# Kernel optimization log

Measured on AMD Instinct MI355X. Metric: run time of the kernel, lower is better.

Reference implementation:

```python
import jax, jax.numpy as jnp
import numpy as np

N = 50000
E = 1600000
NUM_GRAPHS = 64
NEG_SLOPE = 0.2


def _glorot(key, shape):
    fan_in, fan_out = shape[0], shape[-1]
    lim = jnp.sqrt(6.0 / (fan_in + fan_out))
    return jax.random.uniform(key, shape, jnp.float32, -lim, lim)


def setup_inputs() -> dict:
    key = jax.random.key(0)
    ks = jax.random.split(key, 16)
    x = jax.random.normal(ks[0], (N, 128), jnp.float32)
    edge_index = jax.random.randint(ks[1], (2, E), 0, N, jnp.int64)
    batch = jnp.sort(jax.random.randint(ks[2], (N,), 0, NUM_GRAPHS, jnp.int64))
    dims = [(128, 32), (32, 64), (64, 128)]
    params = {}
    for i, (fi, fo) in enumerate(dims, start=1):
        params[f'W{i}'] = _glorot(ks[3 * i], (fi, fo))
        params[f'a_src{i}'] = _glorot(ks[3 * i + 1], (1, fo))[0]
        params[f'a_dst{i}'] = _glorot(ks[3 * i + 2], (1, fo))[0]
        params[f'b{i}'] = jnp.zeros((fo,), jnp.float32)
    params['lin1_W'] = _glorot(ks[12], (128, 32))
    params['lin1_b'] = jnp.zeros((32,), jnp.float32)
    params['lin2_W'] = _glorot(ks[13], (32, 10))
    params['lin2_b'] = jnp.zeros((10,), jnp.float32)
    return dict(x=x, edge_index=edge_index, batch=batch, **params)


def gat_conv(x, src, dst, W, a_src, a_dst, b):
    # h: [N, F_out]
    h = x @ W
    # per-node attention logits, gathered per edge
    as_n = h @ a_src  # [N]
    ad_n = h @ a_dst  # [N]
    e = jax.nn.leaky_relu(as_n[src] + ad_n[dst], NEG_SLOPE)  # [E']
    # segment softmax over incoming edges of each destination node
    m = jax.ops.segment_max(e, dst, num_segments=N)
    ee = jnp.exp(e - m[dst])
    s = jax.ops.segment_sum(ee, dst, num_segments=N)
    alpha = ee / (s[dst] + 1e-16)
    # weighted scatter-add of source messages
    out = jax.ops.segment_sum(h[src] * alpha[:, None], dst, num_segments=N)
    return out + b


def reference(x, edge_index, batch, W1, a_src1, a_dst1, b1, W2, a_src2, a_dst2, b2,
              W3, a_src3, a_dst3, b3, lin1_W, lin1_b, lin2_W, lin2_b):
    # add self loops (PyG GATConv default)
    loops = jnp.arange(N, dtype=edge_index.dtype)
    src = jnp.concatenate([edge_index[0], loops])
    dst = jnp.concatenate([edge_index[1], loops])
    h = jax.nn.relu(gat_conv(x, src, dst, W1, a_src1, a_dst1, b1))
    h = jax.nn.relu(gat_conv(h, src, dst, W2, a_src2, a_dst2, b2))
    h = gat_conv(h, src, dst, W3, a_src3, a_dst3, b3)
    # global_add_pool over graphs
    g = jax.ops.segment_sum(h, batch, num_segments=NUM_GRAPHS)  # [G, 128]
    g = jax.nn.relu(g @ lin1_W + lin1_b)
    g = g @ lin2_W + lin2_b
    # faithful to original: log_softmax over dim=0 (batch axis)
    return jax.nn.log_softmax(g, axis=0)
```

## Files before the change

kernel.cpp:

```cpp
#include <hip/hip_runtime.h>
#include <cstdint>
#include <cstddef>

#define NN 50000
#define NE 1600000
#define NG 64
#define NCB 196
#define EPB_A 16384
#define CAP_B 16384

__device__ __forceinline__ float bflo(unsigned u) { return __uint_as_float(u << 16); }
__device__ __forceinline__ float bfhi(unsigned u) { return __uint_as_float(u & 0xffff0000u); }
__device__ __forceinline__ unsigned f2bf(float f) {
    unsigned u = __float_as_uint(f);
    return (u + 0x7fffu + ((u >> 16) & 1u)) >> 16;
}

template <int FIN, int FOUT>
__global__ void gemm_bf_k(const float* __restrict__ A, const float* __restrict__ W,
                          unsigned* __restrict__ Hb, int n) {
    const int RPB = 32;
    const int CP = FOUT / 2;
    const int CLANES = 256 / CP;
    const int RL = RPB / CLANES;
    __shared__ float Wl[FIN * FOUT];
    __shared__ float Al[RPB * FIN];
    int tid = threadIdx.x;
    for (int i = tid; i < (FIN * FOUT) / 4; i += 256)
        ((float4*)Wl)[i] = ((const float4*)W)[i];
    int rowbase = blockIdx.x * RPB;
    int nrows = min(RPB, n - rowbase);
    int nel4 = (nrows * FIN) / 4;
    const float4* Asrc = (const float4*)(A + (size_t)rowbase * FIN);
    for (int i = tid; i < nel4; i += 256) ((float4*)Al)[i] = Asrc[i];
    __syncthreads();
    int c2 = tid % CP;
    int rb = tid / CP;
    float acc0[RL], acc1[RL];
#pragma unroll
    for (int r = 0; r < RL; ++r) { acc0[r] = 0.f; acc1[r] = 0.f; }
#pragma unroll 4
    for (int k = 0; k < FIN; ++k) {
        float w0 = Wl[k * FOUT + 2 * c2];
        float w1 = Wl[k * FOUT + 2 * c2 + 1];
#pragma unroll
        for (int r = 0; r < RL; ++r) {
            float a = Al[(rb + r * CLANES) * FIN + k];
            acc0[r] += a * w0;
            acc1[r] += a * w1;
        }
    }
#pragma unroll
    for (int r = 0; r < RL; ++r) {
        int row = rowbase + rb + r * CLANES;
        if (row < n) Hb[(size_t)row * CP + c2] = f2bf(acc0[r]) | (f2bf(acc1[r]) << 16);
    }
}

template <int F>
__global__ void att_logits_k(const unsigned short* __restrict__ Hb,
                             const float* __restrict__ a_src, const float* __restrict__ a_dst,
                             float* __restrict__ as_, float* __restrict__ ad_) {
    const int GRP = F / 4;
    long long t = (long long)blockIdx.x * blockDim.x + threadIdx.x;
    int node = (int)(t / GRP);
    int lane = (int)(t % GRP);
    if (node >= NN) return;
    ushort4 h4 = ((const ushort4*)(Hb + (size_t)node * F))[lane];
    float h0 = bflo(h4.x), h1 = bflo(h4.y), h2 = bflo(h4.z), h3 = bflo(h4.w);
    float4 s4 = ((const float4*)a_src)[lane];
    float4 d4 = ((const float4*)a_dst)[lane];
    float s1 = h0 * s4.x + h1 * s4.y + h2 * s4.z + h3 * s4.w;
    float s2 = h0 * d4.x + h1 * d4.y + h2 * d4.z + h3 * d4.w;
#pragma unroll
    for (int o = GRP >> 1; o; o >>= 1) {
        s1 += __shfl_xor(s1, o, GRP);
        s2 += __shfl_xor(s2, o, GRP);
    }
    if (lane == 0) {
        as_[node] = s1;
        ad_[node] = s2;
    }
}

__global__ void chist_k(const int* __restrict__ edst, int* __restrict__ gcount) {
    __shared__ int h[NCB];
    int tid = threadIdx.x;
    for (int i = tid; i < NCB; i += 256) h[i] = 0;
    __syncthreads();
    const int total4 = NE / 4;
    for (int i = blockIdx.x * 256 + tid; i < total4; i += gridDim.x * 256) {
        int4 d = ((const int4*)edst)[i];
        atomicAdd(&h[d.x >> 8], 1);
        atomicAdd(&h[d.y >> 8], 1);
        atomicAdd(&h[d.z >> 8], 1);
        atomicAdd(&h[d.w >> 8], 1);
    }
    __syncthreads();
    for (int i = tid; i < NCB; i += 256)
        if (h[i]) atomicAdd(&gcount[i], h[i]);
}

__global__ void cscan_k(const int* __restrict__ gcount, int* __restrict__ cbase,
                        int* __restrict__ gcur) {
    __shared__ int sc[256];
    int tid = threadIdx.x;
    int c0 = (tid < NCB) ? gcount[tid] : 0;
    sc[tid] = c0;
    __syncthreads();
    for (int off = 1; off < 256; off <<= 1) {
        int v = (tid >= off) ? sc[tid - off] : 0;
        __syncthreads();
        sc[tid] += v;
        __syncthreads();
    }
    int excl = sc[tid] - c0;
    if (tid < NCB) { cbase[tid] = excl; gcur[tid] = excl; }
    if (tid == 255) cbase[NCB] = sc[255];
}

__global__ void parta_k(const int* __restrict__ esrc, const int* __restrict__ edst,
                        int* __restrict__ gcur, int* __restrict__ pk_g) {
    __shared__ int cnt[NCB];
    __shared__ int base[NCB];
    __shared__ int cur[NCB];
    __shared__ int gposs[NCB];
    __shared__ int sc[256];
    __shared__ int lpk[EPB_A];
    int tid = threadIdx.x;
    int e0 = blockIdx.x * EPB_A;
    int e1 = min(e0 + EPB_A, NE);
    for (int i = tid; i < NCB; i += 256) cnt[i] = 0;
    __syncthreads();
    for (int i = e0 / 4 + tid; i < e1 / 4; i += 256) {
        int4 d = ((const int4*)edst)[i];
        atomicAdd(&cnt[d.x >> 8], 1);
        atomicAdd(&cnt[d.y >> 8], 1);
        atomicAdd(&cnt[d.z >> 8], 1);
        atomicAdd(&cnt[d.w >> 8], 1);
    }
    __syncthreads();
    int c0 = (tid < NCB) ? cnt[tid] : 0;
    sc[tid] = c0;
    __syncthreads();
    for (int off = 1; off < 256; off <<= 1) {
        int v = (tid >= off) ? sc[tid - off] : 0;
        __syncthreads();
        sc[tid] += v;
        __syncthreads();
    }
    if (tid < NCB) {
        int excl = sc[tid] - c0;
        base[tid] = excl;
        cur[tid] = excl;
        gposs[tid] = atomicAdd(&gcur[tid], c0);
    }
    __syncthreads();
    for (int i = e0 / 4 + tid; i < e1 / 4; i += 256) {
        int4 d = ((const int4*)edst)[i];
        int4 s = ((const int4*)esrc)[i];
        lpk[atomicAdd(&cur[d.x >> 8], 1)] = s.x | ((d.x & 255) << 17);
        lpk[atomicAdd(&cur[d.y >> 8], 1)] = s.y | ((d.y & 255) << 17);
        lpk[atomicAdd(&cur[d.z >> 8], 1)] = s.z | ((d.z & 255) << 17);
        lpk[atomicAdd(&cur[d.w >> 8], 1)] = s.w | ((d.w & 255) << 17);
    }
    __syncthreads();
    int wid = tid >> 6, lane = tid & 63;
    for (int c = wid; c < NCB; c += 4) {
        int n = cnt[c], gb = gposs[c], lb = base[c];
        for (int i = lane; i < n; i += 64) pk_g[gb + i] = lpk[lb + i];
    }
}

__global__ void partb_k(const int* __restrict__ pk_g, const int* __restrict__ cbase,
                        int* __restrict__ offsets, int* __restrict__ csr) {
    __shared__ int cnt[256];
    __shared__ int sc[256];
    __shared__ int lpk[CAP_B];
    int b = blockIdx.x, tid = threadIdx.x;
    int ebeg = cbase[b], eend = cbase[b + 1], n = eend - ebeg;
    int nbeg = b * 256;
    int ncnt = min(256, NN - nbeg);
    cnt[tid] = 0;
    __syncthreads();
    bool fits = (n <= CAP_B);
    if (fits) {
        for (int i = tid; i < n; i += 256) {
            int p = pk_g[ebeg + i];
            lpk[i] = p;
            atomicAdd(&cnt[p >> 17], 1);
        }
    } else {
        for (int i = tid; i < n; i += 256) atomicAdd(&cnt[pk_g[ebeg + i] >> 17], 1);
    }
    __syncthreads();
    int c0 = cnt[tid];
    sc[tid] = c0;
    __syncthreads();
    for (int off = 1; off < 256; off <<= 1) {
        int v = (tid >= off) ? sc[tid - off] : 0;
        __syncthreads();
        sc[tid] += v;
        __syncthreads();
    }
    int excl = sc[tid] - c0;
    if (tid < ncnt) offsets[nbeg + tid] = ebeg + excl;
    if (b == NCB - 1 && tid == 0) offsets[NN] = eend;
    __syncthreads();
    cnt[tid] = ebeg + excl;
    __syncthreads();
    if (fits) {
        for (int i = tid; i < n; i += 256) {
            int p = lpk[i];
            csr[atomicAdd(&cnt[p >> 17], 1)] = p & 0x1FFFF;
        }
    } else {
        for (int i = tid; i < n; i += 256) {
            int p = pk_g[ebeg + i];
            csr[atomicAdd(&cnt[p >> 17], 1)] = p & 0x1FFFF;
        }
    }
}

template <int F, bool RELU>
__global__ void node_agg_k(const int* __restrict__ off, const int* __restrict__ csr,
                           const float* __restrict__ as_, const float* __restrict__ ad_,
                           const unsigned* __restrict__ Hb2,
                           const float* __restrict__ b, float* __restrict__ O) {
    const int GRP = F / 2;
    const int EPG = 64 / GRP;
    const int U = (EPG == 1) ? 4 : 2;
    int lane = threadIdx.x & 63;
    int node = blockIdx.x * (blockDim.x >> 6) + (threadIdx.x >> 6);
    if (node >= NN) return;
    int beg = off[node], end = off[node + 1];
    float adn = ad_[node];
    float vself = as_[node] + adn;
    vself = vself > 0.f ? vself : 0.2f * vself;

    float mx = vself;
    for (int i = beg + lane; i < end; i += 64) {
        float v = as_[csr[i]] + adn;
        v = v > 0.f ? v : 0.2f * v;
        mx = fmaxf(mx, v);
    }
#pragma unroll
    for (int o = 32; o; o >>= 1) mx = fmaxf(mx, __shfl_xor(mx, o));

    int sg = lane / GRP;
    int cl = lane % GRP;
    float eself = __expf(vself - mx);
    unsigned hbs = Hb2[(size_t)node * GRP + cl];
    float accx = (sg == 0) ? eself * bflo(hbs) : 0.f;
    float accy = (sg == 0) ? eself * bfhi(hbs) : 0.f;
    float lsum = 0.f;

    for (int i0 = beg; i0 < end; i0 += 64) {
        int idx = i0 + lane;
        bool ok = idx < end;
        int s = ok ? csr[idx] : 0;
        float v = as_[s] + adn;
        v = v > 0.f ? v : 0.2f * v;
        float ee = ok ? __expf(v - mx) : 0.f;
        lsum += ee;
        int rem = min(end - i0, 64);
        int nj = (rem + EPG - 1) / EPG;
        nj = (nj + U - 1) & ~(U - 1);
        for (int j = 0; j < nj; j += U) {
#pragma unroll
            for (int k = 0; k < U; ++k) {
                int pos = (j + k) * EPG + sg;
                int s2 = __shfl(s, pos);
                float ee2 = __shfl(ee, pos);
                unsigned hb = Hb2[(size_t)s2 * GRP + cl];
                accx += ee2 * bflo(hb);
                accy += ee2 * bfhi(hb);
            }
        }
    }
#pragma unroll
    for (int o = 32; o; o >>= 1) lsum += __shfl_xor(lsum, o);
    float sum = lsum + eself;
#pragma unroll
    for (int o = 32; o >= GRP; o >>= 1) {
        accx += __shfl_xor(accx, o);
        accy += __shfl_xor(accy, o);
    }
    if (sg == 0) {
        float inv = 1.f / (sum + 1e-16f);
        float2 bb = ((const float2*)b)[cl];
        float ox = accx * inv + bb.x;
        float oy = accy * inv + bb.y;
        if (RELU) {
            ox = fmaxf(ox, 0.f);
            oy = fmaxf(oy, 0.f);
        }
        ((float2*)O)[(size_t)node * GRP + cl] = make_float2(ox, oy);
    }
}

__global__ void pool_k(const float* __restrict__ O, const int* __restrict__ batch,
                       float* __restrict__ g, int nodes_per_block) {
    __shared__ float acc[NG * 128];
    int c = threadIdx.x;
    for (int i = 0; i < NG; ++i) acc[i * 128 + c] = 0.f;
    int start = blockIdx.x * nodes_per_block;
    int end = min(start + nodes_per_block, NN);
    int gmin = NG - 1, gmax = 0;
    for (int nd = start; nd < end; ++nd) {
        int gg = batch[nd];
        gmin = min(gmin, gg);
        gmax = max(gmax, gg);
        acc[gg * 128 + c] += O[(size_t)nd * 128 + c];
    }
    for (int i = gmin; i <= gmax; ++i) atomicAdd(g + i * 128 + c, acc[i * 128 + c]);
}

__global__ void head_k(const float* __restrict__ g, const float* __restrict__ l1W,
                       const float* __restrict__ l1b, const float* __restrict__ l2W,
                       const float* __restrict__ l2b, float* __restrict__ out) {
    __shared__ float h1[NG * 32];
    __shared__ float o[NG * 10];
    int tid = threadIdx.x;
    for (int idx = tid; idx < NG * 32; idx += 256) {
        int r = idx / 32, c = idx % 32;
        float acc = l1b[c];
        for (int k = 0; k < 128; ++k) acc += g[r * 128 + k] * l1W[k * 32 + c];
        h1[idx] = fmaxf(acc, 0.f);
    }
    __syncthreads();
    for (int idx = tid; idx < NG * 10; idx += 256) {
        int r = idx / 10, c = idx % 10;
        float acc = l2b[c];
        for (int k = 0; k < 32; ++k) acc += h1[r * 32 + k] * l2W[k * 10 + c];
        o[idx] = acc;
    }
    __syncthreads();
    if (tid < 10) {
        float mx = -1e30f;
        for (int r = 0; r < NG; ++r) mx = fmaxf(mx, o[r * 10 + tid]);
        float sum = 0.f;
        for (int r = 0; r < NG; ++r) sum += __expf(o[r * 10 + tid] - mx);
        float lse = mx + logf(sum);
        for (int r = 0; r < NG; ++r) out[r * 10 + tid] = o[r * 10 + tid] - lse;
    }
}

extern "C" void kernel_launch(void* const* d_in, const int* in_sizes, int n_in,
                              void* d_out, int out_size, void* d_ws, size_t ws_size,
                              hipStream_t stream) {
    const float* x   = (const float*)d_in[0];
    const int* ei    = (const int*)d_in[1];
    const int* batch = (const int*)d_in[2];
    const float* W1 = (const float*)d_in[3];
    const float* as1 = (const float*)d_in[4];
    const float* ad1 = (const float*)d_in[5];
    const float* b1 = (const float*)d_in[6];
    const float* W2 = (const float*)d_in[7];
    const float* as2 = (const float*)d_in[8];
    const float* ad2 = (const float*)d_in[9];
    const float* b2 = (const float*)d_in[10];
    const float* W3 = (const float*)d_in[11];
    const float* as3 = (const float*)d_in[12];
    const float* ad3 = (const float*)d_in[13];
    const float* b3 = (const float*)d_in[14];
    const float* l1W = (const float*)d_in[15];
    const float* l1b = (const float*)d_in[16];
    const float* l2W = (const float*)d_in[17];
    const float* l2b = (const float*)d_in[18];
    float* out = (float*)d_out;

    const int* esrc = ei;
    const int* edst = ei + NE;

    char* ws = (char*)d_ws;
    float* B0 = (float*)ws;
    float* B1 = B0 + (size_t)NN * 128;
    unsigned* Hb = (unsigned*)(B1 + (size_t)NN * 64);
    float* as_ = (float*)(Hb + (size_t)NN * 64);
    float* ad_ = as_ + NN;
    int* gcount = (int*)(ad_ + NN);
    int* cbase  = gcount + NCB;
    int* gcur   = cbase + NCB + 1;
    int* offsets = gcur + NCB + 2;
    int* csr    = offsets + NN + 1;
    int* pk     = csr + NE;
    float* g    = (float*)(pk + NE);

    hipMemsetAsync(gcount, 0, NCB * 4, stream);
    chist_k<<<98, 256, 0, stream>>>(edst, gcount);
    cscan_k<<<1, 256, 0, stream>>>(gcount, cbase, gcur);
    parta_k<<<(NE + EPB_A - 1) / EPB_A, 256, 0, stream>>>(esrc, edst, gcur, pk);
    partb_k<<<NCB, 256, 0, stream>>>(pk, cbase, offsets, csr);

    gemm_bf_k<128, 32><<<(NN + 31) / 32, 256, 0, stream>>>(x, W1, Hb, NN);
    att_logits_k<32><<<((long long)NN * 8 + 255) / 256, 256, 0, stream>>>(
        (const unsigned short*)Hb, as1, ad1, as_, ad_);
    node_agg_k<32, true><<<(NN + 3) / 4, 256, 0, stream>>>(offsets, csr, as_, ad_, Hb, b1, B0);

    gemm_bf_k<32, 64><<<(NN + 31) / 32, 256, 0, stream>>>(B0, W2, Hb, NN);
    att_logits_k<64><<<((long long)NN * 16 + 255) / 256, 256, 0, stream>>>(
        (const unsigned short*)Hb, as2, ad2, as_, ad_);
    node_agg_k<64, true><<<(NN + 3) / 4, 256, 0, stream>>>(offsets, csr, as_, ad_, Hb, b2, B1);

    gemm_bf_k<64, 128><<<(NN + 31) / 32, 256, 0, stream>>>(B1, W3, Hb, NN);
    att_logits_k<128><<<((long long)NN * 32 + 255) / 256, 256, 0, stream>>>(
        (const unsigned short*)Hb, as3, ad3, as_, ad_);
    node_agg_k<128, false><<<(NN + 3) / 4, 256, 0, stream>>>(offsets, csr, as_, ad_, Hb, b3, B0);

    hipMemsetAsync(g, 0, (size_t)NG * 128 * 4, stream);
    pool_k<<<(NN + 127) / 128, 128, 0, stream>>>(B0, batch, g, 128);
    head_k<<<1, 256, 0, stream>>>(g, l1W, l1b, l2W, l2b, out);
}
```

Baseline: 328.8 us.

## Fuse attention logits into GEMM, merge histogram, rework aggregation lanes

Computes the per-node source and destination attention logits inside the GEMM epilogue using shuffle reductions, which removes the separate att_logits kernels and the re-read of H. The destination histogram is folded into the first GEMM launch as extra blocks, and the two memsets are combined into one by placing g next to gcount. The 64- and 128-feature aggregation paths now have each lane own output columns and broadcast edge indices with readlane, instead of splitting the wavefront into edge subgroups and reducing across them at the end. This trades fewer launches and less memory traffic for a longer serial per-edge loop in each wavefront.

```diff
diff --git a/kernel.cpp b/kernel.cpp
--- a/kernel.cpp
+++ b/kernel.cpp
@@ -15,21 +15,45 @@
     unsigned u = __float_as_uint(f);
     return (u + 0x7fffu + ((u >> 16) & 1u)) >> 16;
 }
-
-template <int FIN, int FOUT>
-__global__ void gemm_bf_k(const float* __restrict__ A, const float* __restrict__ W,
-                          unsigned* __restrict__ Hb, int n) {
+__device__ __forceinline__ float rdlane_f(float v, int l) {
+    return __uint_as_float((unsigned)__builtin_amdgcn_readlane((int)__float_as_uint(v), l));
+}
+
+template <int FIN, int FOUT, bool HIST>
+__global__ void gemm_att_k(const float* __restrict__ A, const float* __restrict__ W,
+                           const float* __restrict__ a_src, const float* __restrict__ a_dst,
+                           unsigned* __restrict__ Hb, float* __restrict__ as_,
+                           float* __restrict__ ad_, int gemmBlocks,
+                           const int* __restrict__ edst, int* __restrict__ gcount) {
+    __shared__ float Wl[FIN * FOUT];
+    __shared__ float Al[32 * FIN];
+    __shared__ int hh[NCB];
+    int tid = threadIdx.x;
+    if (HIST && blockIdx.x >= gemmBlocks) {
+        int bid = blockIdx.x - gemmBlocks;
+        for (int i = tid; i < NCB; i += 256) hh[i] = 0;
+        __syncthreads();
+        const int total4 = NE / 4;
+        for (int i = bid * 256 + tid; i < total4; i += 98 * 256) {
+            int4 d = ((const int4*)edst)[i];
+            atomicAdd(&hh[d.x >> 8], 1);
+            atomicAdd(&hh[d.y >> 8], 1);
+            atomicAdd(&hh[d.z >> 8], 1);
+            atomicAdd(&hh[d.w >> 8], 1);
+        }
+        __syncthreads();
+        for (int i = tid; i < NCB; i += 256)
+            if (hh[i]) atomicAdd(&gcount[i], hh[i]);
+        return;
+    }
     const int RPB = 32;
     const int CP = FOUT / 2;
     const int CLANES = 256 / CP;
     const int RL = RPB / CLANES;
-    __shared__ float Wl[FIN * FOUT];
-    __shared__ float Al[RPB * FIN];
-    int tid = threadIdx.x;
     for (int i = tid; i < (FIN * FOUT) / 4; i += 256)
         ((float4*)Wl)[i] = ((const float4*)W)[i];
     int rowbase = blockIdx.x * RPB;
-    int nrows = min(RPB, n - rowbase);
+    int nrows = min(RPB, NN - rowbase);
     int nel4 = (nrows * FIN) / 4;
     const float4* Asrc = (const float4*)(A + (size_t)rowbase * FIN);
     for (int i = tid; i < nel4; i += 256) ((float4*)Al)[i] = Asrc[i];
@@ -50,55 +74,23 @@
             acc1[r] += a * w1;
         }
     }
+    float2 asrc2 = ((const float2*)a_src)[c2];
+    float2 adst2 = ((const float2*)a_dst)[c2];
 #pragma unroll
     for (int r = 0; r < RL; ++r) {
         int row = rowbase + rb + r * CLANES;
-        if (row < n) Hb[(size_t)row * CP + c2] = f2bf(acc0[r]) | (f2bf(acc1[r]) << 16);
-    }
-}
-
-template <int F>
-__global__ void att_logits_k(const unsigned short* __restrict__ Hb,
-                             const float* __restrict__ a_src, const float* __restrict__ a_dst,
-                             float* __restrict__ as_, float* __restrict__ ad_) {
-    const int GRP = F / 4;
-    long long t = (long long)blockIdx.x * blockDim.x + threadIdx.x;
-    int node = (int)(t / GRP);
-    int lane = (int)(t % GRP);
-    if (node >= NN) return;
-    ushort4 h4 = ((const ushort4*)(Hb + (size_t)node * F))[lane];
-    float h0 = bflo(h4.x), h1 = bflo(h4.y), h2 = bflo(h4.z), h3 = bflo(h4.w);
-    float4 s4 = ((const float4*)a_src)[lane];
-    float4 d4 = ((const float4*)a_dst)[lane];
-    float s1 = h0 * s4.x + h1 * s4.y + h2 * s4.z + h3 * s4.w;
-    float s2 = h0 * d4.x + h1 * d4.y + h2 * d4.z + h3 * d4.w;
-#pragma unroll
-    for (int o = GRP >> 1; o; o >>= 1) {
-        s1 += __shfl_xor(s1, o, GRP);
-        s2 += __shfl_xor(s2, o, GRP);
-    }
-    if (lane == 0) {
-        as_[node] = s1;
-        ad_[node] = s2;
-    }
-}
-
-__global__ void chist_k(const int* __restrict__ edst, int* __restrict__ gcount) {
-    __shared__ int h[NCB];
-    int tid = threadIdx.x;
-    for (int i = tid; i < NCB; i += 256) h[i] = 0;
-    __syncthreads();
-    const int total4 = NE / 4;
-    for (int i = blockIdx.x * 256 + tid; i < total4; i += gridDim.x * 256) {
-        int4 d = ((const int4*)edst)[i];
-        atomicAdd(&h[d.x >> 8], 1);
-        atomicAdd(&h[d.y >> 8], 1);
-        atomicAdd(&h[d.z >> 8], 1);
-        atomicAdd(&h[d.w >> 8], 1);
-    }
-    __syncthreads();
-    for (int i = tid; i < NCB; i += 256)
-        if (h[i]) atomicAdd(&gcount[i], h[i]);
+        float p1 = acc0[r] * asrc2.x + acc1[r] * asrc2.y;
+        float p2 = acc0[r] * adst2.x + acc1[r] * adst2.y;
+#pragma unroll
+        for (int o = CP >> 1; o; o >>= 1) {
+            p1 += __shfl_xor(p1, o, CP);
+            p2 += __shfl_xor(p2, o, CP);
+        }
+        if (row < NN) {
+            Hb[(size_t)row * CP + c2] = f2bf(acc0[r]) | (f2bf(acc1[r]) << 16);
+            if (c2 == 0) { as_[row] = p1; ad_[row] = p2; }
+        }
+    }
 }
 
 __global__ void cscan_k(const int* __restrict__ gcount, int* __restrict__ cbase,
@@ -227,9 +219,6 @@
                            const float* __restrict__ as_, const float* __restrict__ ad_,
                            const unsigned* __restrict__ Hb2,
                            const float* __restrict__ b, float* __restrict__ O) {
-    const int GRP = F / 2;
-    const int EPG = 64 / GRP;
-    const int U = (EPG == 1) ? 4 : 2;
     int lane = threadIdx.x & 63;
     int node = blockIdx.x * (blockDim.x >> 6) + (threadIdx.x >> 6);
     if (node >= NN) return;
@@ -246,56 +235,128 @@
     }
 #pragma unroll
     for (int o = 32; o; o >>= 1) mx = fmaxf(mx, __shfl_xor(mx, o));
-
-    int sg = lane / GRP;
-    int cl = lane % GRP;
     float eself = __expf(vself - mx);
-    unsigned hbs = Hb2[(size_t)node * GRP + cl];
-    float accx = (sg == 0) ? eself * bflo(hbs) : 0.f;
-    float accy = (sg == 0) ? eself * bfhi(hbs) : 0.f;
     float lsum = 0.f;
 
-    for (int i0 = beg; i0 < end; i0 += 64) {
-        int idx = i0 + lane;
-        bool ok = idx < end;
-        int s = ok ? csr[idx] : 0;
-        float v = as_[s] + adn;
-        v = v > 0.f ? v : 0.2f * v;
-        float ee = ok ? __expf(v - mx) : 0.f;
-        lsum += ee;
-        int rem = min(end - i0, 64);
-        int nj = (rem + EPG - 1) / EPG;
-        nj = (nj + U - 1) & ~(U - 1);
-        for (int j = 0; j < nj; j += U) {
-#pragma unroll
-            for (int k = 0; k < U; ++k) {
-                int pos = (j + k) * EPG + sg;
-                int s2 = __shfl(s, pos);
-                float ee2 = __shfl(ee, pos);
-                unsigned hb = Hb2[(size_t)s2 * GRP + cl];
+    if constexpr (F == 128) {
+        unsigned hbs = Hb2[(size_t)node * 64 + lane];
+        float accx = eself * bflo(hbs);
+        float accy = eself * bfhi(hbs);
+        for (int i0 = beg; i0 < end; i0 += 64) {
+            int idx = i0 + lane;
+            bool ok = idx < end;
+            int s = ok ? csr[idx] : 0;
+            float v = as_[s] + adn;
+            v = v > 0.f ? v : 0.2f * v;
+            float ee = ok ? __expf(v - mx) : 0.f;
+            lsum += ee;
+            int rem = min(end - i0, 64);
+            int j = 0;
+            for (; j + 4 <= rem; j += 4) {
+#pragma unroll
+                for (int k = 0; k < 4; ++k) {
+                    int s2 = __builtin_amdgcn_readlane(s, j + k);
+                    float ee2 = rdlane_f(ee, j + k);
+                    unsigned hb = (Hb2 + (size_t)s2 * 64)[lane];
+                    accx += ee2 * bflo(hb);
+                    accy += ee2 * bfhi(hb);
+                }
+            }
+            for (; j < rem; ++j) {
+                int s2 = __builtin_amdgcn_readlane(s, j);
+                float ee2 = rdlane_f(ee, j);
+                unsigned hb = (Hb2 + (size_t)s2 * 64)[lane];
                 accx += ee2 * bflo(hb);
                 accy += ee2 * bfhi(hb);
             }
         }
-    }
-#pragma unroll
-    for (int o = 32; o; o >>= 1) lsum += __shfl_xor(lsum, o);
-    float sum = lsum + eself;
-#pragma unroll
-    for (int o = 32; o >= GRP; o >>= 1) {
-        accx += __shfl_xor(accx, o);
-        accy += __shfl_xor(accy, o);
-    }
-    if (sg == 0) {
-        float inv = 1.f / (sum + 1e-16f);
-        float2 bb = ((const float2*)b)[cl];
+#pragma unroll
+        for (int o = 32; o; o >>= 1) lsum += __shfl_xor(lsum, o);
+        float inv = 1.f / (lsum + eself + 1e-16f);
+        float2 bb = ((const float2*)b)[lane];
         float ox = accx * inv + bb.x;
         float oy = accy * inv + bb.y;
-        if (RELU) {
-            ox = fmaxf(ox, 0.f);
-            oy = fmaxf(oy, 0.f);
-        }
-        ((float2*)O)[(size_t)node * GRP + cl] = make_float2(ox, oy);
+        if (RELU) { ox = fmaxf(ox, 0.f); oy = fmaxf(oy, 0.f); }
+        ((float2*)O)[(size_t)node * 64 + lane] = make_float2(ox, oy);
+    } else if constexpr (F == 64) {
+        const unsigned short* Hs = (const unsigned short*)Hb2;
+        float acc = eself * bflo((unsigned)Hs[(size_t)node * 64 + lane]);
+        for (int i0 = beg; i0 < end; i0 += 64) {
+            int idx = i0 + lane;
+            bool ok = idx < end;
+            int s = ok ? csr[idx] : 0;
+            float v = as_[s] + adn;
+            v = v > 0.f ? v : 0.2f * v;
+            float ee = ok ? __expf(v - mx) : 0.f;
+            lsum += ee;
+            int rem = min(end - i0, 64);
+            int j = 0;
+            for (; j + 4 <= rem; j += 4) {
+#pragma unroll
+                for (int k = 0; k < 4; ++k) {
+                    int s2 = __builtin_amdgcn_readlane(s, j + k);
+                    float ee2 = rdlane_f(ee, j + k);
+                    acc += ee2 * bflo((unsigned)(Hs + (size_t)s2 * 64)[lane]);
+                }
+            }
+            for (; j < rem; ++j) {
+                int s2 = __builtin_amdgcn_readlane(s, j);
+                float ee2 = rdlane_f(ee, j);
+                acc += ee2 * bflo((unsigned)(Hs + (size_t)s2 * 64)[lane]);
+            }
+        }
+#pragma unroll
+        for (int o = 32; o; o >>= 1) lsum += __shfl_xor(lsum, o);
+        float inv = 1.f / (lsum + eself + 1e-16f);
+        float ox = acc * inv + b[lane];
+        if (RELU) ox = fmaxf(ox, 0.f);
+        O[(size_t)node * 64 + lane] = ox;
+    } else {
+        const int GRP = 16, EPG = 4, U = 2;
+        int sg = lane / GRP;
+        int cl = lane % GRP;
+        unsigned hbs = Hb2[(size_t)node * GRP + cl];
+        float accx = (sg == 0) ? eself * bflo(hbs) : 0.f;
+        float accy = (sg == 0) ? eself * bfhi(hbs) : 0.f;
+        for (int i0 = beg; i0 < end; i0 += 64) {
+            int idx = i0 + lane;
+            bool ok = idx < end;
+            int s = ok ? csr[idx] : 0;
+            float v = as_[s] + adn;
+            v = v > 0.f ? v : 0.2f * v;
+            float ee = ok ? __expf(v - mx) : 0.f;
+            lsum += ee;
+            int rem = min(end - i0, 64);
+            int nj = (rem + EPG - 1) / EPG;
+            nj = (nj + U - 1) & ~(U - 1);
+            for (int j = 0; j < nj; j += U) {
+#pragma unroll
+                for (int k = 0; k < U; ++k) {
+                    int pos = (j + k) * EPG + sg;
+                    int s2 = __shfl(s, pos);
+                    float ee2 = __shfl(ee, pos);
+                    unsigned hb = Hb2[(size_t)s2 * GRP + cl];
+                    accx += ee2 * bflo(hb);
+                    accy += ee2 * bfhi(hb);
+                }
+            }
+        }
+#pragma unroll
+        for (int o = 32; o; o >>= 1) lsum += __shfl_xor(lsum, o);
+        float sum = lsum + eself;
+#pragma unroll
+        for (int o = 32; o >= GRP; o >>= 1) {
+            accx += __shfl_xor(accx, o);
+            accy += __shfl_xor(accy, o);
+        }
+        if (sg == 0) {
+            float inv = 1.f / (sum + 1e-16f);
+            float2 bb = ((const float2*)b)[cl];
+            float ox = accx * inv + bb.x;
+            float oy = accy * inv + bb.y;
+            if (RELU) { ox = fmaxf(ox, 0.f); oy = fmaxf(oy, 0.f); }
+            ((float2*)O)[(size_t)node * GRP + cl] = make_float2(ox, oy);
+        }
     }
 }
 
@@ -380,35 +441,31 @@
     float* as_ = (float*)(Hb + (size_t)NN * 64);
     float* ad_ = as_ + NN;
     int* gcount = (int*)(ad_ + NN);
-    int* cbase  = gcount + NCB;
+    float* g    = (float*)(gcount + NCB);
+    int* cbase  = (int*)(g + NG * 128);
     int* gcur   = cbase + NCB + 1;
     int* offsets = gcur + NCB + 2;
     int* csr    = offsets + NN + 1;
     int* pk     = csr + NE;
-    float* g    = (float*)(pk + NE);
-
-    hipMemsetAsync(gcount, 0, NCB * 4, stream);
-    chist_k<<<98, 256, 0, stream>>>(edst, gcount);
+    const int GEMM_BLOCKS = (NN + 31) / 32;
+
+    hipMemsetAsync(gcount, 0, (NCB + NG * 128) * 4, stream);
+
+    gemm_att_k<128, 32, true><<<GEMM_BLOCKS + 98, 256, 0, stream>>>(
+        x, W1, as1, ad1, Hb, as_, ad_, GEMM_BLOCKS, edst, gcount);
     cscan_k<<<1, 256, 0, stream>>>(gcount, cbase, gcur);
     parta_k<<<(NE + EPB_A - 1) / EPB_A, 256, 0, stream>>>(esrc, edst, gcur, pk);
     partb_k<<<NCB, 256, 0, stream>>>(pk, cbase, offsets, csr);
-
-    gemm_bf_k<128, 32><<<(NN + 31) / 32, 256, 0, stream>>>(x, W1, Hb, NN);
-    att_logits_k<32><<<((long long)NN * 8 + 255) / 256, 256, 0, stream>>>(
-        (const unsigned short*)Hb, as1, ad1, as_, ad_);
     node_agg_k<32, true><<<(NN + 3) / 4, 256, 0, stream>>>(offsets, csr, as_, ad_, Hb, b1, B0);
 
-    gemm_bf_k<32, 64><<<(NN + 31) / 32, 256, 0, stream>>>(B0, W2, Hb, NN);
-    att_logits_k<64><<<((long long)NN * 16 + 255) / 256, 256, 0, stream>>>(
-        (const unsigned short*)Hb, as2, ad2, as_, ad_);
+    gemm_att_k<32, 64, false><<<GEMM_BLOCKS, 256, 0, stream>>>(
+        B0, W2, as2, ad2, Hb, as_, ad_, GEMM_BLOCKS, nullptr, nullptr);
     node_agg_k<64, true><<<(NN + 3) / 4, 256, 0, stream>>>(offsets, csr, as_, ad_, Hb, b2, B1);
 
-    gemm_bf_k<64, 128><<<(NN + 31) / 32, 256, 0, stream>>>(B1, W3, Hb, NN);
-    att_logits_k<128><<<((long long)NN * 32 + 255) / 256, 256, 0, stream>>>(
-        (const unsigned short*)Hb, as3, ad3, as_, ad_);
+    gemm_att_k<64, 128, false><<<GEMM_BLOCKS, 256, 0, stream>>>(
+        B1, W3, as3, ad3, Hb, as_, ad_, GEMM_BLOCKS, nullptr, nullptr);
     node_agg_k<128, false><<<(NN + 3) / 4, 256, 0, stream>>>(offsets, csr, as_, ad_, Hb, b3, B0);
 
-    hipMemsetAsync(g, 0, (size_t)NG * 128 * 4, stream);
     pool_k<<<(NN + 127) / 128, 128, 0, stream>>>(B0, batch, g, 128);
     head_k<<<1, 256, 0, stream>>>(g, l1W, l1b, l2W, l2b, out);
 }
```

New measurement: 325.9 us. No clear change (-0.9%).
